# Performance work log

Measured on AMD Instinct MI355X. Metric: run time of the kernel, lower is better.

The kernel has to match this reference:

```python
import jax, jax.numpy as jnp
import numpy as np

D_MODEL = 1024
N_HEADS = 16


def setup_inputs() -> dict:
    key = jax.random.key(0)
    ks = jax.random.split(key, 11)
    B, S, D = 2, 2048, D_MODEL
    scale = 1.0 / np.sqrt(D)
    inp = {
        "q": jax.random.normal(ks[0], (B, S, D), jnp.float32),
        "k": jax.random.normal(ks[1], (B, S, D), jnp.float32),
        "v": jax.random.normal(ks[2], (B, S, D), jnp.float32),
        "W_q": jax.random.normal(ks[3], (D, D), jnp.float32) * scale,
        "b_q": jnp.zeros((D,), jnp.float32),
        "W_k": jax.random.normal(ks[4], (D, D), jnp.float32) * scale,
        "b_k": jnp.zeros((D,), jnp.float32),
        "W_v": jax.random.normal(ks[5], (D, D), jnp.float32) * scale,
        "b_v": jnp.zeros((D,), jnp.float32),
        "W_o": jax.random.normal(ks[6], (D, D), jnp.float32) * scale,
        "b_o": jnp.zeros((D,), jnp.float32),
    }
    return inp


def reference(q, k, v, W_q, b_q, W_k, b_k, W_v, b_v, W_o, b_o):
    B, S, D = q.shape
    H = N_HEADS
    d_k = D // H
    # linear projections, then split heads: [B, H, S, d_k]
    def proj(x, W, b):
        y = jnp.einsum("bsd,de->bse", x, W.T) + b
        return y.reshape(B, S, H, d_k).transpose(0, 2, 1, 3)
    Q = proj(q, W_q, b_q)
    K = proj(k, W_k, b_k)
    V = proj(v, W_v, b_v)
    # scaled dot-product attention with explicit [B,H,S,S] scores
    scores = jnp.einsum("bhqd,bhkd->bhqk", Q, K) / jnp.sqrt(jnp.float32(d_k))
    attn = jax.nn.softmax(scores, axis=-1)
    out = jnp.einsum("bhqk,bhkd->bhqd", attn, V)
    out = out.transpose(0, 2, 1, 3).reshape(B, S, D)
    return jnp.einsum("bsd,de->bse", out, W_o.T) + b_o
```

## Files before the change

### kernel.cpp

```cpp
#include <hip/hip_runtime.h>
#include <hip/hip_bf16.h>
#include <math.h>

typedef __bf16 bf16_t;
typedef bf16_t bf16x8 __attribute__((ext_vector_type(8)));
typedef float f32x4 __attribute__((ext_vector_type(4)));

#define D_MODEL 1024
#define NH 16
#define DK 64
#define SEQ 2048
#define MROWS 4096
#define LDSW 64
#define LDC 136

__device__ __forceinline__ bf16x8 ldfrag(const bf16_t* p) {
    union { uint4 u; bf16x8 v; } c;
    c.u = *reinterpret_cast<const uint4*>(p);
    return c.v;
}

__device__ __forceinline__ f32x4 zero4() { f32x4 z = {0.f, 0.f, 0.f, 0.f}; return z; }

__device__ __forceinline__ void gll16(const bf16_t* g, bf16_t* l) {
    __builtin_amdgcn_global_load_lds(
        (const __attribute__((address_space(1))) unsigned int*)g,
        (__attribute__((address_space(3))) unsigned int*)l,
        16, 0, 0);
}

__global__ void pack7(const float* __restrict__ q, const float* __restrict__ k,
                      const float* __restrict__ v, const float* __restrict__ wq,
                      const float* __restrict__ wk, const float* __restrict__ wv,
                      const float* __restrict__ wo,
                      bf16_t* __restrict__ dq, bf16_t* __restrict__ dk,
                      bf16_t* __restrict__ dv, bf16_t* __restrict__ dwq,
                      bf16_t* __restrict__ dwk, bf16_t* __restrict__ dwv,
                      bf16_t* __restrict__ dwo) {
    const int y = blockIdx.y;
    if (y >= 3 && blockIdx.x >= 1024) return;
    const float* s;
    bf16_t* d;
    switch (y) {
        case 0: s = q;  d = dq;  break;
        case 1: s = k;  d = dk;  break;
        case 2: s = v;  d = dv;  break;
        case 3: s = wq; d = dwq; break;
        case 4: s = wk; d = dwk; break;
        case 5: s = wv; d = dwv; break;
        default: s = wo; d = dwo; break;
    }
    int i = (blockIdx.x * blockDim.x + threadIdx.x) * 4;
    float4 f = *reinterpret_cast<const float4*>(s + i);
    union { bf16_t h[4]; uint2 u; } o;
    o.h[0] = (bf16_t)f.x; o.h[1] = (bf16_t)f.y; o.h[2] = (bf16_t)f.z; o.h[3] = (bf16_t)f.w;
    *reinterpret_cast<uint2*>(d + i) = o.u;
}

__device__ __forceinline__ void gemm_core(
    const bf16_t* __restrict__ A, const bf16_t* __restrict__ Bm,
    int K, int m0, int n0,
    bf16_t* As, bf16_t* Bs,
    f32x4 acc[4][4]) {

    const int tid = threadIdx.x;
    const int lane = tid & 63;
    const int wid = tid >> 6;
    const int wm = (wid >> 1) * 64, wn = (wid & 1) * 64;
    const int l15 = lane & 15, quad = lane >> 4;

    const int lrow   = lane >> 3;
    const int gcol   = ((lane & 7) ^ lrow) * 8;

    #pragma unroll
    for (int i = 0; i < 4; i++)
        #pragma unroll
        for (int j = 0; j < 4; j++) acc[i][j] = zero4();

    for (int k0 = 0; k0 < K; k0 += 64) {
        __syncthreads();
        #pragma unroll
        for (int t = 0; t < 4; t++) {
            const int rbase = wid * 32 + t * 8;
            gll16(A  + (size_t)(m0 + rbase + lrow) * K + k0 + gcol, As + rbase * LDSW);
            gll16(Bm + (size_t)(n0 + rbase + lrow) * K + k0 + gcol, Bs + rbase * LDSW);
        }
        __syncthreads();
        #pragma unroll
        for (int c = 0; c < 2; c++) {
            bf16x8 af[4], bfr[4];
            #pragma unroll
            for (int i = 0; i < 4; i++) {
                const int row = wm + i * 16 + l15;
                const int pc = ((c * 4 + quad) ^ (l15 & 7)) * 8;
                af[i] = ldfrag(As + row * LDSW + pc);
            }
            #pragma unroll
            for (int j = 0; j < 4; j++) {
                const int row = wn + j * 16 + l15;
                const int pc = ((c * 4 + quad) ^ (l15 & 7)) * 8;
                bfr[j] = ldfrag(Bs + row * LDSW + pc);
            }
            #pragma unroll
            for (int i = 0; i < 4; i++)
                #pragma unroll
                for (int j = 0; j < 4; j++)
                    acc[i][j] = __builtin_amdgcn_mfma_f32_16x16x32_bf16(af[i], bfr[j], acc[i][j], 0, 0, 0);
        }
    }
}

__global__ __launch_bounds__(256, 3) void proj_gemm(
    const bf16_t* __restrict__ qb, const bf16_t* __restrict__ kb,
    const bf16_t* __restrict__ vb,
    const bf16_t* __restrict__ Wq, const bf16_t* __restrict__ Wk,
    const bf16_t* __restrict__ Wv,
    const float* __restrict__ bq, const float* __restrict__ bk, const float* __restrict__ bv,
    bf16_t* __restrict__ Qh, bf16_t* __restrict__ Kh, bf16_t* __restrict__ Vt) {

    __shared__ __align__(16) bf16_t sm[128 * LDC];
    bf16_t* As = sm;
    bf16_t* Bs = sm + 128 * LDSW;
    bf16_t (*Cs)[LDC] = reinterpret_cast<bf16_t(*)[LDC]>(sm);
    f32x4 acc[4][4];

    const int mode = blockIdx.z;
    const bf16_t* X = (mode == 0) ? qb : (mode == 1) ? kb : vb;
    const bf16_t* W = (mode == 0) ? Wq : (mode == 1) ? Wk : Wv;
    const float* bias = (mode == 0) ? bq : (mode == 1) ? bk : bv;
    const int m0 = blockIdx.y * 128, n0 = blockIdx.x * 128;

    gemm_core(X, W, D_MODEL, m0, n0, As, Bs, acc);

    const int tid = threadIdx.x, lane = tid & 63, wid = tid >> 6;
    const int wm = (wid >> 1) * 64, wn = (wid & 1) * 64;
    const int l15 = lane & 15, quad = lane >> 4;

    __syncthreads();
    if (mode != 2) {
        const float sc = (mode == 0) ? 0.125f * 1.44269504f : 1.0f;
        #pragma unroll
        for (int i = 0; i < 4; i++)
            #pragma unroll
            for (int j = 0; j < 4; j++)
                #pragma unroll
                for (int r = 0; r < 4; r++) {
                    int gn = n0 + wn + j * 16 + l15;
                    Cs[wm + i * 16 + quad * 4 + r][wn + j * 16 + l15] =
                        (bf16_t)((acc[i][j][r] + bias[gn]) * sc);
                }
    } else {
        #pragma unroll
        for (int i = 0; i < 4; i++)
            #pragma unroll
            for (int j = 0; j < 4; j++)
                #pragma unroll
                for (int r = 0; r < 4; r++) {
                    int gn = n0 + wn + j * 16 + l15;
                    Cs[wn + j * 16 + l15][wm + i * 16 + quad * 4 + r] =
                        (bf16_t)(acc[i][j][r] + bias[gn]);
                }
    }
    __syncthreads();

    #pragma unroll
    for (int c = tid; c < 2048; c += 256) {
        int row = c >> 4, col8 = (c & 15) << 3;
        uint4 val = *reinterpret_cast<const uint4*>(&Cs[row][col8]);
        if (mode != 2) {
            int gm = m0 + row, gn = n0 + col8;
            int b = gm >> 11, seq = gm & 2047;
            int h = gn >> 6, dk = gn & 63;
            bf16_t* dst = (mode == 0) ? Qh : Kh;
            *reinterpret_cast<uint4*>(dst + ((size_t)(b * NH + h) * SEQ + seq) * DK + dk) = val;
        } else {
            int gn = n0 + row, gm = m0 + col8;
            int b = gm >> 11, seq = gm & 2047;
            int h = gn >> 6, dk = gn & 63;
            *reinterpret_cast<uint4*>(Vt + ((size_t)(b * NH + h) * DK + dk) * SEQ + seq) = val;
        }
    }
}

__global__ __launch_bounds__(256, 2) void out_gemm(
    const bf16_t* __restrict__ Oc, const bf16_t* __restrict__ Wo,
    const float* __restrict__ bo, float* __restrict__ Cout) {

    __shared__ __align__(16) bf16_t As[64 * LDSW];
    __shared__ __align__(16) bf16_t Bs[128 * LDSW];
    f32x4 acc[2][4];
    const int m0 = blockIdx.y * 64, n0 = blockIdx.x * 128;

    const int tid = threadIdx.x;
    const int lane = tid & 63;
    const int wid = tid >> 6;
    const int wm = (wid >> 1) * 32, wn = (wid & 1) * 64;
    const int l15 = lane & 15, quad = lane >> 4;
    const int lrow = lane >> 3;
    const int gcol = ((lane & 7) ^ lrow) * 8;

    #pragma unroll
    for (int i = 0; i < 2; i++)
        #pragma unroll
        for (int j = 0; j < 4; j++) acc[i][j] = zero4();

    for (int k0 = 0; k0 < D_MODEL; k0 += 64) {
        __syncthreads();
        #pragma unroll
        for (int t = 0; t < 2; t++) {
            const int rbase = wid * 16 + t * 8;
            gll16(Oc + (size_t)(m0 + rbase + lrow) * D_MODEL + k0 + gcol, As + rbase * LDSW);
        }
        #pragma unroll
        for (int t = 0; t < 4; t++) {
            const int rbase = wid * 32 + t * 8;
            gll16(Wo + (size_t)(n0 + rbase + lrow) * D_MODEL + k0 + gcol, Bs + rbase * LDSW);
        }
        __syncthreads();
        #pragma unroll
        for (int c = 0; c < 2; c++) {
            bf16x8 af[2], bfr[4];
            #pragma unroll
            for (int i = 0; i < 2; i++) {
                const int row = wm + i * 16 + l15;
                const int pc = ((c * 4 + quad) ^ (l15 & 7)) * 8;
                af[i] = ldfrag(As + row * LDSW + pc);
            }
            #pragma unroll
            for (int j = 0; j < 4; j++) {
                const int row = wn + j * 16 + l15;
                const int pc = ((c * 4 + quad) ^ (l15 & 7)) * 8;
                bfr[j] = ldfrag(Bs + row * LDSW + pc);
            }
            #pragma unroll
            for (int i = 0; i < 2; i++)
                #pragma unroll
                for (int j = 0; j < 4; j++)
                    acc[i][j] = __builtin_amdgcn_mfma_f32_16x16x32_bf16(af[i], bfr[j], acc[i][j], 0, 0, 0);
        }
    }

    #pragma unroll
    for (int i = 0; i < 2; i++)
        #pragma unroll
        for (int j = 0; j < 4; j++)
            #pragma unroll
            for (int r = 0; r < 4; r++) {
                int gm = m0 + wm + i * 16 + quad * 4 + r;
                int gn = n0 + wn + j * 16 + l15;
                Cout[(size_t)gm * D_MODEL + gn] = acc[i][j][r] + bo[gn];
            }
}

__global__ __launch_bounds__(256) void attn_kernel(
    const bf16_t* __restrict__ Qh, const bf16_t* __restrict__ Kh,
    const bf16_t* __restrict__ Vt, bf16_t* __restrict__ Oc) {

    __shared__ __align__(16) bf16_t Ks[64 * LDSW];
    __shared__ __align__(16) bf16_t Vts[64 * LDSW];
    __shared__ __align__(16) bf16_t Pls[64 * LDSW];

    const int tid = threadIdx.x, lane = tid & 63, wid = tid >> 6;
    const int l15 = lane & 15, quad = lane >> 4;
    const int bh = blockIdx.x;
    const int q0 = blockIdx.y * 64;
    const bf16_t* Qbase = Qh + (size_t)bh * SEQ * DK;
    const bf16_t* Kbase = Kh + (size_t)bh * SEQ * DK;
    const bf16_t* Vbase = Vt + (size_t)bh * DK * SEQ;

    const int lrow = lane >> 3;
    const int gcol = ((lane & 7) ^ lrow) * 8;

    bf16x8 aQ[2];
    #pragma unroll
    for (int c = 0; c < 2; c++)
        aQ[c] = ldfrag(Qbase + (size_t)(q0 + wid * 16 + l15) * DK + c * 32 + quad * 8);

    f32x4 oacc[4];
    #pragma unroll
    for (int j = 0; j < 4; j++) oacc[j] = zero4();
    float l_acc = 0.f;

    const int s7 = l15 & 7;

    for (int kt = 0; kt < SEQ / 64; kt++) {
        const int k0 = kt * 64;
        __syncthreads();
        #pragma unroll
        for (int t = 0; t < 2; t++) {
            const int rbase = wid * 16 + t * 8;
            const int srow = rbase + lrow;
            const int sigma = ((srow >> 5) << 5) | (((srow >> 2) & 3) << 3) |
                              (((srow >> 4) & 1) << 2) | (srow & 3);
            gll16(Kbase + (size_t)(k0 + sigma) * DK + gcol,      Ks  + rbase * LDSW);
            gll16(Vbase + (size_t)(rbase + lrow) * SEQ + k0 + gcol, Vts + rbase * LDSW);
        }
        __syncthreads();

        f32x4 sacc[4];
        #pragma unroll
        for (int j = 0; j < 4; j++) sacc[j] = zero4();
        #pragma unroll
        for (int c = 0; c < 2; c++) {
            bf16x8 bk4[4];
            #pragma unroll
            for (int j = 0; j < 4; j++) {
                const int pc = ((c * 4 + quad) ^ s7) * 8;
                bk4[j] = ldfrag(Ks + (j * 16 + l15) * LDSW + pc);
            }
            #pragma unroll
            for (int j = 0; j < 4; j++)
                sacc[j] = __builtin_amdgcn_mfma_f32_16x16x32_bf16(
                    bk4[j], aQ[c], sacc[j], 0, 0, 0);
        }

        bf16x8 pb[2];
        #pragma unroll
        for (int c = 0; c < 2; c++) {
            union { bf16_t h[8]; bf16x8 v; } pk;
            #pragma unroll
            for (int half = 0; half < 2; half++) {
                const int j = c * 2 + half;
                float e0 = exp2f(sacc[j][0]);
                float e1 = exp2f(sacc[j][1]);
                float e2 = exp2f(sacc[j][2]);
                float e3 = exp2f(sacc[j][3]);
                l_acc += (e0 + e1) + (e2 + e3);
                pk.h[half * 4 + 0] = (bf16_t)e0;
                pk.h[half * 4 + 1] = (bf16_t)e1;
                pk.h[half * 4 + 2] = (bf16_t)e2;
                pk.h[half * 4 + 3] = (bf16_t)e3;
            }
            pb[c] = pk.v;
        }

        #pragma unroll
        for (int c = 0; c < 2; c++) {
            bf16x8 av[4];
            #pragma unroll
            for (int j = 0; j < 4; j++) {
                const int pc = ((c * 4 + quad) ^ s7) * 8;
                av[j] = ldfrag(Vts + (j * 16 + l15) * LDSW + pc);
            }
            #pragma unroll
            for (int j = 0; j < 4; j++)
                oacc[j] = __builtin_amdgcn_mfma_f32_16x16x32_bf16(
                    av[j], pb[c], oacc[j], 0, 0, 0);
        }
    }

    float l = l_acc;
    l += __shfl_xor(l, 16, 64);
    l += __shfl_xor(l, 32, 64);
    const float inv = 1.0f / l;

    bf16_t* orow = Pls + (wid * 16 + l15) * LDSW;
    #pragma unroll
    for (int jp = 0; jp < 4; jp++) {
        union { bf16_t h[4]; unsigned long long u; } pk;
        pk.h[0] = (bf16_t)(oacc[jp][0] * inv);
        pk.h[1] = (bf16_t)(oacc[jp][1] * inv);
        pk.h[2] = (bf16_t)(oacc[jp][2] * inv);
        pk.h[3] = (bf16_t)(oacc[jp][3] * inv);
        const int Lc = jp * 2 + (quad >> 1);
        *reinterpret_cast<unsigned long long*>(
            orow + ((Lc ^ s7) << 3) + ((quad & 1) << 2)) = pk.u;
    }
    __syncthreads();

    const int b = bh >> 4, h = bh & 15;
    #pragma unroll
    for (int c = tid; c < 512; c += 256) {
        int row = c >> 3, chunk = c & 7;
        uint4 val = *reinterpret_cast<const uint4*>(
            Pls + row * LDSW + ((chunk ^ (row & 7)) << 3));
        *reinterpret_cast<uint4*>(Oc + ((size_t)(b * SEQ + q0 + row)) * D_MODEL + h * DK + (chunk << 3)) = val;
    }
}

extern "C" void kernel_launch(void* const* d_in, const int* in_sizes, int n_in,
                              void* d_out, int out_size, void* d_ws, size_t ws_size,
                              hipStream_t stream) {
    const float* q  = (const float*)d_in[0];
    const float* k  = (const float*)d_in[1];
    const float* v  = (const float*)d_in[2];
    const float* Wq = (const float*)d_in[3];
    const float* bq = (const float*)d_in[4];
    const float* Wk = (const float*)d_in[5];
    const float* bk = (const float*)d_in[6];
    const float* Wv = (const float*)d_in[7];
    const float* bv = (const float*)d_in[8];
    const float* Wo = (const float*)d_in[9];
    const float* bo = (const float*)d_in[10];

    const size_t nx = (size_t)MROWS * D_MODEL;
    const size_t nw = (size_t)D_MODEL * D_MODEL;

    bf16_t* qb  = (bf16_t*)d_ws;
    bf16_t* kb  = qb  + nx;
    bf16_t* vb  = kb  + nx;
    bf16_t* Wqb = vb  + nx;
    bf16_t* Wkb = Wqb + nw;
    bf16_t* Wvb = Wkb + nw;
    bf16_t* Wob = Wvb + nw;
    bf16_t* Qh  = Wob + nw;
    bf16_t* Kh  = Qh  + nx;
    bf16_t* Vt  = Kh  + nx;
    bf16_t* Oc  = Vt  + nx;

    pack7<<<dim3(4096, 7), 256, 0, stream>>>(q, k, v, Wq, Wk, Wv, Wo,
                                             qb, kb, vb, Wqb, Wkb, Wvb, Wob);

    proj_gemm<<<dim3(8, 32, 3), 256, 0, stream>>>(qb, kb, vb, Wqb, Wkb, Wvb, bq, bk, bv, Qh, Kh, Vt);
    attn_kernel<<<dim3(32, 32), 256, 0, stream>>>(Qh, Kh, Vt, Oc);
    out_gemm<<<dim3(8, 64), 256, 0, stream>>>(Oc, Wob, bo, (float*)d_out);
}
```

Before: 235.1 us.

## Double attention KV tile to 128 keys and widen pack conversion to 8 elements

The attention kernel now processes 128 keys per iteration instead of 64. This halves the number of barrier pairs and loop iterations, at the cost of larger LDS tiles (32 KB, with the output staging buffer aliased onto the K tile behind an extra barrier) and more score registers. The V tile uses a new 16-way XOR swizzle to match its 128-wide rows, and launch bounds request 4 blocks per CU. Separately, the fp32-to-bf16 pack kernel converts 8 elements per thread with 16-byte stores, halving its grid.

After: 222.8 us. 1.06x faster.

```diff
diff --git a/kernel.cpp b/kernel.cpp
--- a/kernel.cpp
+++ b/kernel.cpp
@@ -38,7 +38,7 @@
                       bf16_t* __restrict__ dwk, bf16_t* __restrict__ dwv,
                       bf16_t* __restrict__ dwo) {
     const int y = blockIdx.y;
-    if (y >= 3 && blockIdx.x >= 1024) return;
+    if (y >= 3 && blockIdx.x >= 512) return;
     const float* s;
     bf16_t* d;
     switch (y) {
@@ -50,11 +50,13 @@
         case 5: s = wv; d = dwv; break;
         default: s = wo; d = dwo; break;
     }
-    int i = (blockIdx.x * blockDim.x + threadIdx.x) * 4;
-    float4 f = *reinterpret_cast<const float4*>(s + i);
-    union { bf16_t h[4]; uint2 u; } o;
-    o.h[0] = (bf16_t)f.x; o.h[1] = (bf16_t)f.y; o.h[2] = (bf16_t)f.z; o.h[3] = (bf16_t)f.w;
-    *reinterpret_cast<uint2*>(d + i) = o.u;
+    int i = (blockIdx.x * blockDim.x + threadIdx.x) * 8;
+    float4 f0 = *reinterpret_cast<const float4*>(s + i);
+    float4 f1 = *reinterpret_cast<const float4*>(s + i + 4);
+    union { bf16_t h[8]; uint4 u; } o;
+    o.h[0] = (bf16_t)f0.x; o.h[1] = (bf16_t)f0.y; o.h[2] = (bf16_t)f0.z; o.h[3] = (bf16_t)f0.w;
+    o.h[4] = (bf16_t)f1.x; o.h[5] = (bf16_t)f1.y; o.h[6] = (bf16_t)f1.z; o.h[7] = (bf16_t)f1.w;
+    *reinterpret_cast<uint4*>(d + i) = o.u;
 }
 
 __device__ __forceinline__ void gemm_core(
@@ -252,13 +254,14 @@
             }
 }
 
-__global__ __launch_bounds__(256) void attn_kernel(
+__global__ __launch_bounds__(256, 4) void attn_kernel(
     const bf16_t* __restrict__ Qh, const bf16_t* __restrict__ Kh,
     const bf16_t* __restrict__ Vt, bf16_t* __restrict__ Oc) {
 
-    __shared__ __align__(16) bf16_t Ks[64 * LDSW];
-    __shared__ __align__(16) bf16_t Vts[64 * LDSW];
-    __shared__ __align__(16) bf16_t Pls[64 * LDSW];
+    __shared__ __align__(16) bf16_t sma[16384];
+    bf16_t* Ks  = sma;
+    bf16_t* Vts = sma + 128 * 64;
+    bf16_t* Pls = sma;
 
     const int tid = threadIdx.x, lane = tid & 63, wid = tid >> 6;
     const int l15 = lane & 15, quad = lane >> 4;
@@ -282,41 +285,47 @@
     float l_acc = 0.f;
 
     const int s7 = l15 & 7;
-
-    for (int kt = 0; kt < SEQ / 64; kt++) {
-        const int k0 = kt * 64;
-        __syncthreads();
-        #pragma unroll
-        for (int t = 0; t < 2; t++) {
-            const int rbase = wid * 16 + t * 8;
+    const int vlrow = lane >> 4;
+    const int vchk0 = lane & 15;
+
+    for (int kt = 0; kt < SEQ / 128; kt++) {
+        const int k0 = kt * 128;
+        __syncthreads();
+        #pragma unroll
+        for (int t = 0; t < 4; t++) {
+            const int rbase = wid * 32 + t * 8;
             const int srow = rbase + lrow;
             const int sigma = ((srow >> 5) << 5) | (((srow >> 2) & 3) << 3) |
                               (((srow >> 4) & 1) << 2) | (srow & 3);
-            gll16(Kbase + (size_t)(k0 + sigma) * DK + gcol,      Ks  + rbase * LDSW);
-            gll16(Vbase + (size_t)(rbase + lrow) * SEQ + k0 + gcol, Vts + rbase * LDSW);
-        }
-        __syncthreads();
-
-        f32x4 sacc[4];
-        #pragma unroll
-        for (int j = 0; j < 4; j++) sacc[j] = zero4();
+            gll16(Kbase + (size_t)(k0 + sigma) * DK + gcol, Ks + rbase * 64);
+
+            const int vrb = wid * 16 + t * 4;
+            const int vrow = vrb + vlrow;
+            gll16(Vbase + (size_t)vrow * SEQ + k0 + ((vchk0 ^ (vrow & 15)) << 3),
+                  Vts + vrb * 128);
+        }
+        __syncthreads();
+
+        f32x4 sacc[8];
+        #pragma unroll
+        for (int j = 0; j < 8; j++) sacc[j] = zero4();
         #pragma unroll
         for (int c = 0; c < 2; c++) {
-            bf16x8 bk4[4];
-            #pragma unroll
-            for (int j = 0; j < 4; j++) {
+            bf16x8 bk4[8];
+            #pragma unroll
+            for (int j = 0; j < 8; j++) {
                 const int pc = ((c * 4 + quad) ^ s7) * 8;
-                bk4[j] = ldfrag(Ks + (j * 16 + l15) * LDSW + pc);
-            }
-            #pragma unroll
-            for (int j = 0; j < 4; j++)
+                bk4[j] = ldfrag(Ks + (j * 16 + l15) * 64 + pc);
+            }
+            #pragma unroll
+            for (int j = 0; j < 8; j++)
                 sacc[j] = __builtin_amdgcn_mfma_f32_16x16x32_bf16(
                     bk4[j], aQ[c], sacc[j], 0, 0, 0);
         }
 
-        bf16x8 pb[2];
-        #pragma unroll
-        for (int c = 0; c < 2; c++) {
+        bf16x8 pb[4];
+        #pragma unroll
+        for (int c = 0; c < 4; c++) {
             union { bf16_t h[8]; bf16x8 v; } pk;
             #pragma unroll
             for (int half = 0; half < 2; half++) {
@@ -335,12 +344,12 @@
         }
 
         #pragma unroll
-        for (int c = 0; c < 2; c++) {
+        for (int c = 0; c < 4; c++) {
             bf16x8 av[4];
             #pragma unroll
             for (int j = 0; j < 4; j++) {
-                const int pc = ((c * 4 + quad) ^ s7) * 8;
-                av[j] = ldfrag(Vts + (j * 16 + l15) * LDSW + pc);
+                const int pc = ((c * 4 + quad) ^ l15) * 8;
+                av[j] = ldfrag(Vts + (j * 16 + l15) * 128 + pc);
             }
             #pragma unroll
             for (int j = 0; j < 4; j++)
@@ -353,6 +362,8 @@
     l += __shfl_xor(l, 16, 64);
     l += __shfl_xor(l, 32, 64);
     const float inv = 1.0f / l;
+
+    __syncthreads();
 
     bf16_t* orow = Pls + (wid * 16 + l15) * LDSW;
     #pragma unroll
@@ -408,7 +419,7 @@
     bf16_t* Vt  = Kh  + nx;
     bf16_t* Oc  = Vt  + nx;
 
-    pack7<<<dim3(4096, 7), 256, 0, stream>>>(q, k, v, Wq, Wk, Wv, Wo,
+    pack7<<<dim3(2048, 7), 256, 0, stream>>>(q, k, v, Wq, Wk, Wv, Wo,
                                              qb, kb, vb, Wqb, Wkb, Wvb, Wob);
 
     proj_gemm<<<dim3(8, 32, 3), 256, 0, stream>>>(qb, kb, vb, Wqb, Wkb, Wvb, bq, bk, bv, Qh, Kh, Vt);
```
